# Kernel optimization log

Hardware: AMD Instinct MI355X
Metric: run time of the kernel (lower is better)

## Reference

```python
import jax, jax.numpy as jnp
import numpy as np
import math

N = 8192        # n_cells
D_IN = 512      # input_dim
D_H = 1024      # hidden_dim
N_F = 8         # min(8, N//2)
FS = N // N_F   # faction size
SYNC = 0.15
DEBATE = 0.15
TWO_PI = 2.0 * math.pi


def setup_inputs() -> dict:
    key = jax.random.key(0)
    ks = jax.random.split(key, 10)
    phases = jax.random.uniform(ks[0], (N,), dtype=jnp.float32) * TWO_PI
    omegas = jax.random.normal(ks[1], (N,), dtype=jnp.float32) * 0.5 + 1.0
    coupling = jax.random.normal(ks[2], (N, N), dtype=jnp.float32) * 0.01
    K = jnp.asarray(2.0, dtype=jnp.float32)
    # Linear weights stored as [in, out]
    w_p2h = jax.random.normal(ks[3], (2, D_H), dtype=jnp.float32) * (1.0 / math.sqrt(2.0))
    b_p2h = jnp.zeros((D_H,), dtype=jnp.float32)
    w_enc1 = jax.random.normal(ks[4], (D_H + D_IN, D_H), dtype=jnp.float32) * (1.0 / math.sqrt(D_H + D_IN))
    b_enc1 = jnp.zeros((D_H,), dtype=jnp.float32)
    w_enc2 = jax.random.normal(ks[5], (D_H, D_H), dtype=jnp.float32) * (1.0 / math.sqrt(D_H))
    b_enc2 = jnp.zeros((D_H,), dtype=jnp.float32)
    w_out = jax.random.normal(ks[6], (D_H, D_IN), dtype=jnp.float32) * (1.0 / math.sqrt(D_H))
    b_out = jnp.zeros((D_IN,), dtype=jnp.float32)
    x = jax.random.normal(ks[7], (D_IN,), dtype=jnp.float32)
    return {"x": x, "phases": phases, "omegas": omegas, "coupling": coupling, "K": K,
            "w_p2h": w_p2h, "b_p2h": b_p2h, "w_enc1": w_enc1, "b_enc1": b_enc1,
            "w_enc2": w_enc2, "b_enc2": b_enc2, "w_out": w_out, "b_out": b_out,
            "step": 10}


def _forward(x, phases, omegas, coupling, K, w_p2h, b_p2h, w_enc1, b_enc1,
             w_enc2, b_enc2, w_out, b_out, step):
    # --- kuramoto_step (torch runs it under no_grad) ---
    input_mag = jax.lax.stop_gradient(jnp.linalg.norm(x))
    phase_diff = phases[:, None] - phases[None, :]                 # [N, N]
    coupling_eff = jax.nn.sigmoid(coupling) * K / N                # [N, N]
    interactions = (coupling_eff * jnp.sin(phase_diff)).sum(axis=1)
    dtheta = omegas + interactions + input_mag * 0.1
    phases_new = jax.lax.stop_gradient((phases + 0.1 * dtheta) % TWO_PI)
    sin_p, cos_p = jnp.sin(phases_new), jnp.cos(phases_new)
    r = jnp.sqrt(cos_p.mean() ** 2 + sin_p.mean() ** 2)
    tension = jnp.abs(r - 0.5) * 2.0                               # scalar (non-diff, .item() in torch)

    # --- phase features -> per-cell hidden ---
    phase_features = jnp.stack([sin_p, cos_p], axis=-1)            # [N, 2]
    cell_hiddens = phase_features @ w_p2h + b_p2h                  # [N, D_H]

    # --- faction_sync_debate, vectorized over the 8 factions ---
    h = cell_hiddens.reshape(N_F, FS, D_H)
    fmean = h.mean(axis=1, keepdims=True)                          # [N_F, 1, D_H]
    h = (1.0 - SYNC) * h + SYNC * fmean
    if step > 5:  # step is a static Python int
        global_opinion = h.mean(axis=1).mean(axis=0)               # [D_H]
        dc = max(1, FS // 4)
        h = h.at[:, :dc].set((1.0 - DEBATE) * h[:, :dc] + DEBATE * global_opinion)
    cell_hiddens = h.reshape(N, D_H)

    # --- encode with broadcast input ---
    x_b = jnp.broadcast_to(x, (N, D_IN))
    combined = jnp.concatenate([cell_hiddens, x_b], axis=-1)       # [N, D_H + D_IN]
    encoded = jnp.tanh(combined @ w_enc1 + b_enc1) @ w_enc2 + b_enc2

    # --- coherence-weighted readout ---
    mean_phase = jnp.arctan2(sin_p.mean(), cos_p.mean())
    coherence = jnp.cos(phases_new - mean_phase)                   # [N]
    weights = jax.nn.softmax(coherence * 5.0)
    weighted = (weights[:, None] * encoded).sum(axis=0, keepdims=True)  # [1, D_H]
    output = weighted @ w_out + b_out                              # [1, D_IN]
    return output, tension


def reference(x, phases, omegas, coupling, K, w_p2h, b_p2h, w_enc1, b_enc1,
              w_enc2, b_enc2, w_out, b_out, step):
    return _forward(x, phases, omegas, coupling, K, w_p2h, b_p2h, w_enc1,
                    b_enc1, w_enc2, b_enc2, w_out, b_out, step)
```

## Files before the change

### kernel.cpp

```cpp
#include <hip/hip_runtime.h>
#include <math.h>


#define NC   8192
#define DH   1024
#define DIN  512

using f4 = __attribute__((ext_vector_type(4))) float;

constexpr int IMG = 0, SBAR = 1, CBAR = 2, MPC = 3, MPS = 4, DEN = 5, TENS = 6;
constexpr int SFO = 8, CFO = 16;
constexpr int SN0 = 32;
constexpr int CN0 = SN0 + NC;
constexpr int SNN = CN0 + NC;
constexpr int CNN = SNN + NC;
constexpr int UPART  = CNN + NC;
constexpr int UFIN   = UPART + 16 * 3 * DH;
constexpr int TPART  = UFIN + 3 * DH;
constexpr int W2PART = TPART + 128 * DH;
constexpr int OPART  = W2PART + 16 * DH;

__device__ __forceinline__ float frcp(float x) { return __builtin_amdgcn_rcpf(x); }
__device__ __forceinline__ float sigm(float x) { return frcp(1.f + __expf(-x)); }
__device__ __forceinline__ float ftanh(float x) { return 1.f - 2.f * frcp(__expf(2.f * x) + 1.f); }

template <int BS>
__device__ __forceinline__ float block_reduce(float v, float* sh) {
  #pragma unroll
  for (int m = 1; m < 64; m <<= 1) v += __shfl_xor(v, m, 64);
  constexpr int NW = BS / 64;
  int lane = threadIdx.x & 63, w = threadIdx.x >> 6;
  if (lane == 0) sh[w] = v;
  __syncthreads();
  if (w == 0) {
    float x = (lane < NW) ? sh[lane] : 0.f;
    #pragma unroll
    for (int m = 1; m < NW; m <<= 1) x += __shfl_xor(x, m, 64);
    if (lane == 0) sh[0] = x;
  }
  __syncthreads();
  float r = sh[0];
  __syncthreads();
  return r;
}

__global__ __launch_bounds__(256) void k_prep_up(const float* __restrict__ phases,
                                                 const float* __restrict__ x,
                                                 const float* __restrict__ w_p2h,
                                                 const float* __restrict__ b_p2h,
                                                 const float* __restrict__ w_enc1,
                                                 const float* __restrict__ b_enc1,
                                                 float* __restrict__ W) {
  __shared__ float sh[4];
  int b = blockIdx.x, t = threadIdx.x;
  if (b < 32) {
    int i = b * 256 + t;
    float s, c;
    sincosf(phases[i], &s, &c);
    W[SN0 + i] = s;
    W[CN0 + i] = c;
  } else if (b == 32) {
    float x0 = x[t], x1 = x[t + 256];
    float v = block_reduce<256>(x0 * x0 + x1 * x1, sh);
    if (t == 0) W[IMG] = sqrtf(v);
  } else {
    int idx = b - 33;
    int hb = idx & 3;
    int dy = idx >> 2;
    int h = hb * 256 + t;
    float a0 = 0.f, a1 = 0.f, a2 = 0.f;
    for (int d = dy * 64; d < dy * 64 + 64; ++d) {
      float r = w_enc1[d * DH + h];
      a0 = fmaf(w_p2h[d], r, a0);
      a1 = fmaf(w_p2h[DH + d], r, a1);
      a2 = fmaf(b_p2h[d], r, a2);
    }
    for (int k = dy * 32; k < dy * 32 + 32; ++k)
      a2 = fmaf(x[k], w_enc1[(DH + k) * DH + h], a2);
    if (dy == 0) a2 += b_enc1[h];
    float* up = W + UPART + dy * 3 * DH;
    up[h] = a0;
    up[DH + h] = a1;
    up[2 * DH + h] = a2;
  }
}

__global__ __launch_bounds__(256) void k_rows(const float* __restrict__ coupling,
                                              const float* __restrict__ phases,
                                              const float* __restrict__ omegas,
                                              const float* __restrict__ Kp,
                                              float* __restrict__ W) {
  __shared__ float sh[4][4];
  int t = threadIdx.x;
  int row0 = blockIdx.x * 2;
  const f4* c0 = (const f4*)(coupling + (size_t)row0 * NC);
  const f4* c1 = (const f4*)(coupling + (size_t)(row0 + 1) * NC);
  const f4* s4 = (const f4*)(W + SN0);
  const f4* c4 = (const f4*)(W + CN0);
  float sc0 = 0.f, ss0 = 0.f, sc1 = 0.f, ss1 = 0.f;
  #pragma unroll 4
  for (int k = 0; k < 8; ++k) {
    int idx = k * 256 + t;
    f4 cc = c4[idx];
    f4 sv = s4[idx];
    f4 v0 = __builtin_nontemporal_load(c0 + idx);
    f4 v1 = __builtin_nontemporal_load(c1 + idx);
    #pragma unroll
    for (int e = 0; e < 4; ++e) {
      float g0 = sigm(v0[e]);
      sc0 = fmaf(g0, cc[e], sc0);
      ss0 = fmaf(g0, sv[e], ss0);
      float g1 = sigm(v1[e]);
      sc1 = fmaf(g1, cc[e], sc1);
      ss1 = fmaf(g1, sv[e], ss1);
    }
  }
  #pragma unroll
  for (int m = 1; m < 64; m <<= 1) {
    sc0 += __shfl_xor(sc0, m, 64);
    ss0 += __shfl_xor(ss0, m, 64);
    sc1 += __shfl_xor(sc1, m, 64);
    ss1 += __shfl_xor(ss1, m, 64);
  }
  int lane = t & 63, w = t >> 6;
  if (lane == 0) { sh[w][0] = sc0; sh[w][1] = ss0; sh[w][2] = sc1; sh[w][3] = ss1; }
  __syncthreads();
  if (t < 2) {
    float sc = sh[0][2 * t] + sh[1][2 * t] + sh[2][2 * t] + sh[3][2 * t];
    float ss = sh[0][2 * t + 1] + sh[1][2 * t + 1] + sh[2][2 * t + 1] + sh[3][2 * t + 1];
    int row = row0 + t;
    float kk = Kp[0];
    float si = W[SN0 + row], ci = W[CN0 + row];
    float inter = (kk / (float)NC) * (si * sc - ci * ss);
    float dtheta = omegas[row] + inter + 0.1f * W[IMG];
    float pn = phases[row] + 0.1f * dtheta;
    float s, c;
    sincosf(pn, &s, &c);
    W[SNN + row] = s;
    W[CNN + row] = c;
  }
}

__global__ __launch_bounds__(1024) void k_stats_ured(float* __restrict__ W) {
  if (blockIdx.x > 0) {
    int j = (blockIdx.x - 1) * 1024 + threadIdx.x;
    float v = 0.f;
    #pragma unroll
    for (int p = 0; p < 16; ++p) v += W[UPART + p * 3 * DH + j];
    W[UFIN + j] = v;
    return;
  }
  __shared__ float shS[16], shC[16], shD[16], shMP[2];
  int t = threadIdx.x, lane = t & 63, w = t >> 6;
  int f = w >> 1, half = w & 1;
  int base = f * 1024 + half * 512;
  float s = 0.f, c = 0.f;
  #pragma unroll
  for (int k = 0; k < 8; ++k) {
    int i = base + k * 64 + lane;
    s += W[SNN + i];
    c += W[CNN + i];
  }
  #pragma unroll
  for (int m = 1; m < 64; m <<= 1) {
    s += __shfl_xor(s, m, 64);
    c += __shfl_xor(c, m, 64);
  }
  if (lane == 0) { shS[w] = s; shC[w] = c; }
  __syncthreads();
  if (t == 0) {
    float ssum = 0.f, csum = 0.f;
    #pragma unroll
    for (int ff = 0; ff < 8; ++ff) {
      float S = shS[2 * ff] + shS[2 * ff + 1];
      float C = shC[2 * ff] + shC[2 * ff + 1];
      W[SFO + ff] = S * (1.f / 1024.f);
      W[CFO + ff] = C * (1.f / 1024.f);
      ssum += S;
      csum += C;
    }
    float sbar = ssum * (1.f / (float)NC);
    float cbar = csum * (1.f / (float)NC);
    float mp = atan2f(sbar, cbar);
    float mpc = cosf(mp), mps = sinf(mp);
    W[SBAR] = sbar; W[CBAR] = cbar; W[MPC] = mpc; W[MPS] = mps;
    float r = sqrtf(cbar * cbar + sbar * sbar);
    W[TENS] = fabsf(r - 0.5f) * 2.f;
    shMP[0] = mpc; shMP[1] = mps;
  }
  __syncthreads();
  float mpc = shMP[0], mps = shMP[1];
  float d = 0.f;
  #pragma unroll
  for (int k = 0; k < 8; ++k) {
    int i = k * 1024 + t;
    float coh = W[CNN + i] * mpc + W[SNN + i] * mps;
    d += __expf(5.f * coh - 5.f);
  }
  #pragma unroll
  for (int m = 1; m < 64; m <<= 1) d += __shfl_xor(d, m, 64);
  if (lane == 0) shD[w] = d;
  __syncthreads();
  if (t == 0) {
    float D = 0.f;
    #pragma unroll
    for (int ww = 0; ww < 16; ++ww) D += shD[ww];
    W[DEN] = D;
  }
}

__global__ __launch_bounds__(256) void k_cells(const int* __restrict__ step,
                                               float* __restrict__ W) {
  int t = threadIdx.x, b = blockIdx.x;
  float u0[4], u1[4], u2[4], acc[4] = {0.f, 0.f, 0.f, 0.f};
  #pragma unroll
  for (int k = 0; k < 4; ++k) {
    int h = t + k * 256;
    u0[k] = W[UFIN + h];
    u1[k] = W[UFIN + DH + h];
    u2[k] = W[UFIN + 2 * DH + h];
  }
  bool debate = step[0] > 5;
  float sbar = W[SBAR], cbar = W[CBAR], mpc = W[MPC], mps = W[MPS];
  float invden = 1.0f / W[DEN];
  int i0 = b * 64;
  int f = i0 >> 10;
  float Sf = W[SFO + f], Cf = W[CFO + f];
  bool deb = debate && ((i0 & 1023) < 256);
  for (int j = 0; j < 64; ++j) {
    int i = i0 + j;
    float s = W[SNN + i], c = W[CNN + i];
    float a = fmaf(0.15f, Sf, 0.85f * s);
    float bb = fmaf(0.15f, Cf, 0.85f * c);
    if (deb) {
      a = fmaf(0.15f, sbar, 0.85f * a);
      bb = fmaf(0.15f, cbar, 0.85f * bb);
    }
    float coh = c * mpc + s * mps;
    float wgt = __expf(5.f * coh - 5.f) * invden;
    #pragma unroll
    for (int k = 0; k < 4; ++k) {
      float pre = fmaf(a, u0[k], fmaf(bb, u1[k], u2[k]));
      acc[k] = fmaf(wgt, ftanh(pre), acc[k]);
    }
  }
  #pragma unroll
  for (int k = 0; k < 4; ++k) W[TPART + b * DH + t + k * 256] = acc[k];
}

__global__ __launch_bounds__(256) void k_wv(const float* __restrict__ w_enc2,
                                            const float* __restrict__ b_enc2,
                                            float* __restrict__ W) {
  __shared__ float ts[64];
  int t = threadIdx.x, cb = blockIdx.x, hb = blockIdx.y;
  if (t < 64) {
    int h = hb * 64 + t;
    float v = 0.f;
    for (int p = 0; p < 128; ++p) v += W[TPART + p * DH + h];
    ts[t] = v;
  }
  __syncthreads();
  int c = cb * 256 + t;
  float acc = (hb == 0) ? b_enc2[c] : 0.f;
  #pragma unroll 8
  for (int j = 0; j < 64; ++j) acc = fmaf(ts[j], w_enc2[(hb * 64 + j) * DH + c], acc);
  W[W2PART + hb * DH + c] = acc;
}

__global__ __launch_bounds__(256) void k_out(const float* __restrict__ w_out,
                                             float* __restrict__ W) {
  __shared__ float wv[64];
  int t = threadIdx.x, ob = blockIdx.x, cb = blockIdx.y;
  if (t < 64) {
    int c = cb * 64 + t;
    float v = 0.f;
    #pragma unroll
    for (int p = 0; p < 16; ++p) v += W[W2PART + p * DH + c];
    wv[t] = v;
  }
  __syncthreads();
  int o = ob * 256 + t;
  float acc = 0.f;
  #pragma unroll 8
  for (int j = 0; j < 64; ++j) acc = fmaf(wv[j], w_out[(cb * 64 + j) * DIN + o], acc);
  W[OPART + cb * DIN + o] = acc;
}

__global__ __launch_bounds__(256) void k_final(const float* __restrict__ b_out,
                                               float* __restrict__ W,
                                               float* __restrict__ out) {
  int o = blockIdx.x * 256 + threadIdx.x;
  float acc = b_out[o];
  #pragma unroll
  for (int p = 0; p < 16; ++p) acc += W[OPART + p * DIN + o];
  out[o] = acc;
  if (o == 0) out[DIN] = W[TENS];
}

extern "C" void kernel_launch(void* const* d_in, const int* in_sizes, int n_in,
                              void* d_out, int out_size, void* d_ws, size_t ws_size,
                              hipStream_t stream) {
  (void)in_sizes; (void)n_in; (void)out_size; (void)ws_size;
  const float* x        = (const float*)d_in[0];
  const float* phases   = (const float*)d_in[1];
  const float* omegas   = (const float*)d_in[2];
  const float* coupling = (const float*)d_in[3];
  const float* Kp       = (const float*)d_in[4];
  const float* w_p2h    = (const float*)d_in[5];
  const float* b_p2h    = (const float*)d_in[6];
  const float* w_enc1   = (const float*)d_in[7];
  const float* b_enc1   = (const float*)d_in[8];
  const float* w_enc2   = (const float*)d_in[9];
  const float* b_enc2   = (const float*)d_in[10];
  const float* w_out    = (const float*)d_in[11];
  const float* b_out    = (const float*)d_in[12];
  const int*   step     = (const int*)d_in[13];
  float* W   = (float*)d_ws;
  float* out = (float*)d_out;

  k_prep_up   <<<97, 256, 0, stream>>>(phases, x, w_p2h, b_p2h, w_enc1, b_enc1, W);
  k_rows      <<<NC / 2, 256, 0, stream>>>(coupling, phases, omegas, Kp, W);
  k_stats_ured<<<4, 1024, 0, stream>>>(W);
  k_cells     <<<128, 256, 0, stream>>>(step, W);
  k_wv        <<<dim3(4, 16), 256, 0, stream>>>(w_enc2, b_enc2, W);
  k_out       <<<dim3(2, 16), 256, 0, stream>>>(w_out, W);
  k_final     <<<2, 256, 0, stream>>>(b_out, W, out);
}
```

Baseline: 88.86 us.

## Merge stats kernel into cells, fold weight prep into row pass, 8 rows per block

Removes the separate stats/u-reduction kernel. Every k_cells block now redundantly computes the faction sums, mean phase and softmax denominator over all 8192 cells, and sums the 16 u partials itself. The precomputation of w_enc1 projections moves from the prep kernel into the coupling-row kernel as 64 extra blocks, so it runs alongside the main memory-bound pass. The row kernel now handles 8 rows per block instead of 2, reusing the sin/cos vector loads across rows. This cuts one launch and a serial single-block stage, at the cost of redundant reductions in 128 blocks and higher register pressure in the row kernel.

Measured after the change: 108.1 us. 1.22x slower.

```diff
diff --git a/kernel.cpp b/kernel.cpp
--- a/kernel.cpp
+++ b/kernel.cpp
@@ -8,15 +8,13 @@
 
 using f4 = __attribute__((ext_vector_type(4))) float;
 
-constexpr int IMG = 0, SBAR = 1, CBAR = 2, MPC = 3, MPS = 4, DEN = 5, TENS = 6;
-constexpr int SFO = 8, CFO = 16;
+constexpr int IMG = 0, TENS = 6;
 constexpr int SN0 = 32;
 constexpr int CN0 = SN0 + NC;
 constexpr int SNN = CN0 + NC;
 constexpr int CNN = SNN + NC;
 constexpr int UPART  = CNN + NC;
-constexpr int UFIN   = UPART + 16 * 3 * DH;
-constexpr int TPART  = UFIN + 3 * DH;
+constexpr int TPART  = UPART + 16 * 3 * DH;
 constexpr int W2PART = TPART + 128 * DH;
 constexpr int OPART  = W2PART + 16 * DH;
 
@@ -24,33 +22,9 @@
 __device__ __forceinline__ float sigm(float x) { return frcp(1.f + __expf(-x)); }
 __device__ __forceinline__ float ftanh(float x) { return 1.f - 2.f * frcp(__expf(2.f * x) + 1.f); }
 
-template <int BS>
-__device__ __forceinline__ float block_reduce(float v, float* sh) {
-  #pragma unroll
-  for (int m = 1; m < 64; m <<= 1) v += __shfl_xor(v, m, 64);
-  constexpr int NW = BS / 64;
-  int lane = threadIdx.x & 63, w = threadIdx.x >> 6;
-  if (lane == 0) sh[w] = v;
-  __syncthreads();
-  if (w == 0) {
-    float x = (lane < NW) ? sh[lane] : 0.f;
-    #pragma unroll
-    for (int m = 1; m < NW; m <<= 1) x += __shfl_xor(x, m, 64);
-    if (lane == 0) sh[0] = x;
-  }
-  __syncthreads();
-  float r = sh[0];
-  __syncthreads();
-  return r;
-}
-
-__global__ __launch_bounds__(256) void k_prep_up(const float* __restrict__ phases,
-                                                 const float* __restrict__ x,
-                                                 const float* __restrict__ w_p2h,
-                                                 const float* __restrict__ b_p2h,
-                                                 const float* __restrict__ w_enc1,
-                                                 const float* __restrict__ b_enc1,
-                                                 float* __restrict__ W) {
+__global__ __launch_bounds__(256) void k_prep(const float* __restrict__ phases,
+                                              const float* __restrict__ x,
+                                              float* __restrict__ W) {
   __shared__ float sh[4];
   int b = blockIdx.x, t = threadIdx.x;
   if (b < 32) {
@@ -59,12 +33,31 @@
     sincosf(phases[i], &s, &c);
     W[SN0 + i] = s;
     W[CN0 + i] = c;
-  } else if (b == 32) {
+  } else {
     float x0 = x[t], x1 = x[t + 256];
-    float v = block_reduce<256>(x0 * x0 + x1 * x1, sh);
-    if (t == 0) W[IMG] = sqrtf(v);
-  } else {
-    int idx = b - 33;
+    float v = x0 * x0 + x1 * x1;
+    #pragma unroll
+    for (int m = 1; m < 64; m <<= 1) v += __shfl_xor(v, m, 64);
+    int lane = t & 63, w = t >> 6;
+    if (lane == 0) sh[w] = v;
+    __syncthreads();
+    if (t == 0) W[IMG] = sqrtf(sh[0] + sh[1] + sh[2] + sh[3]);
+  }
+}
+
+__global__ __launch_bounds__(256) void k_rows_up(const float* __restrict__ coupling,
+                                                 const float* __restrict__ phases,
+                                                 const float* __restrict__ omegas,
+                                                 const float* __restrict__ Kp,
+                                                 const float* __restrict__ x,
+                                                 const float* __restrict__ w_p2h,
+                                                 const float* __restrict__ b_p2h,
+                                                 const float* __restrict__ w_enc1,
+                                                 const float* __restrict__ b_enc1,
+                                                 float* __restrict__ W) {
+  int t = threadIdx.x;
+  if (blockIdx.x < 64) {
+    int idx = blockIdx.x;
     int hb = idx & 3;
     int dy = idx >> 2;
     int h = hb * 256 + t;
@@ -82,56 +75,52 @@
     up[h] = a0;
     up[DH + h] = a1;
     up[2 * DH + h] = a2;
-  }
-}
-
-__global__ __launch_bounds__(256) void k_rows(const float* __restrict__ coupling,
-                                              const float* __restrict__ phases,
-                                              const float* __restrict__ omegas,
-                                              const float* __restrict__ Kp,
-                                              float* __restrict__ W) {
-  __shared__ float sh[4][4];
-  int t = threadIdx.x;
-  int row0 = blockIdx.x * 2;
-  const f4* c0 = (const f4*)(coupling + (size_t)row0 * NC);
-  const f4* c1 = (const f4*)(coupling + (size_t)(row0 + 1) * NC);
+    return;
+  }
+  __shared__ float sh[4][16];
+  int row0 = (blockIdx.x - 64) * 8;
+  const f4* cbase = (const f4*)(coupling + (size_t)row0 * NC);
   const f4* s4 = (const f4*)(W + SN0);
   const f4* c4 = (const f4*)(W + CN0);
-  float sc0 = 0.f, ss0 = 0.f, sc1 = 0.f, ss1 = 0.f;
-  #pragma unroll 4
+  float sc[8], ss[8];
+  #pragma unroll
+  for (int r = 0; r < 8; ++r) { sc[r] = 0.f; ss[r] = 0.f; }
   for (int k = 0; k < 8; ++k) {
     int idx = k * 256 + t;
     f4 cc = c4[idx];
     f4 sv = s4[idx];
-    f4 v0 = __builtin_nontemporal_load(c0 + idx);
-    f4 v1 = __builtin_nontemporal_load(c1 + idx);
-    #pragma unroll
-    for (int e = 0; e < 4; ++e) {
-      float g0 = sigm(v0[e]);
-      sc0 = fmaf(g0, cc[e], sc0);
-      ss0 = fmaf(g0, sv[e], ss0);
-      float g1 = sigm(v1[e]);
-      sc1 = fmaf(g1, cc[e], sc1);
-      ss1 = fmaf(g1, sv[e], ss1);
-    }
-  }
-  #pragma unroll
-  for (int m = 1; m < 64; m <<= 1) {
-    sc0 += __shfl_xor(sc0, m, 64);
-    ss0 += __shfl_xor(ss0, m, 64);
-    sc1 += __shfl_xor(sc1, m, 64);
-    ss1 += __shfl_xor(ss1, m, 64);
+    #pragma unroll
+    for (int r = 0; r < 8; ++r) {
+      f4 v = __builtin_nontemporal_load(cbase + r * (NC / 4) + idx);
+      #pragma unroll
+      for (int e = 0; e < 4; ++e) {
+        float g = sigm(v[e]);
+        sc[r] = fmaf(g, cc[e], sc[r]);
+        ss[r] = fmaf(g, sv[e], ss[r]);
+      }
+    }
   }
   int lane = t & 63, w = t >> 6;
-  if (lane == 0) { sh[w][0] = sc0; sh[w][1] = ss0; sh[w][2] = sc1; sh[w][3] = ss1; }
-  __syncthreads();
-  if (t < 2) {
-    float sc = sh[0][2 * t] + sh[1][2 * t] + sh[2][2 * t] + sh[3][2 * t];
-    float ss = sh[0][2 * t + 1] + sh[1][2 * t + 1] + sh[2][2 * t + 1] + sh[3][2 * t + 1];
+  #pragma unroll
+  for (int r = 0; r < 8; ++r) {
+    #pragma unroll
+    for (int m = 1; m < 64; m <<= 1) {
+      sc[r] += __shfl_xor(sc[r], m, 64);
+      ss[r] += __shfl_xor(ss[r], m, 64);
+    }
+  }
+  if (lane == 0) {
+    #pragma unroll
+    for (int r = 0; r < 8; ++r) { sh[w][2 * r] = sc[r]; sh[w][2 * r + 1] = ss[r]; }
+  }
+  __syncthreads();
+  if (t < 8) {
+    float scf = sh[0][2 * t] + sh[1][2 * t] + sh[2][2 * t] + sh[3][2 * t];
+    float ssf = sh[0][2 * t + 1] + sh[1][2 * t + 1] + sh[2][2 * t + 1] + sh[3][2 * t + 1];
     int row = row0 + t;
     float kk = Kp[0];
     float si = W[SN0 + row], ci = W[CN0 + row];
-    float inter = (kk / (float)NC) * (si * sc - ci * ss);
+    float inter = (kk / (float)NC) * (si * scf - ci * ssf);
     float dtheta = omegas[row] + inter + 0.1f * W[IMG];
     float pn = phases[row] + 0.1f * dtheta;
     float s, c;
@@ -141,91 +130,94 @@
   }
 }
 
-__global__ __launch_bounds__(1024) void k_stats_ured(float* __restrict__ W) {
-  if (blockIdx.x > 0) {
-    int j = (blockIdx.x - 1) * 1024 + threadIdx.x;
-    float v = 0.f;
-    #pragma unroll
-    for (int p = 0; p < 16; ++p) v += W[UPART + p * 3 * DH + j];
-    W[UFIN + j] = v;
-    return;
-  }
-  __shared__ float shS[16], shC[16], shD[16], shMP[2];
-  int t = threadIdx.x, lane = t & 63, w = t >> 6;
-  int f = w >> 1, half = w & 1;
-  int base = f * 1024 + half * 512;
-  float s = 0.f, c = 0.f;
-  #pragma unroll
-  for (int k = 0; k < 8; ++k) {
-    int i = base + k * 64 + lane;
-    s += W[SNN + i];
-    c += W[CNN + i];
-  }
-  #pragma unroll
-  for (int m = 1; m < 64; m <<= 1) {
-    s += __shfl_xor(s, m, 64);
-    c += __shfl_xor(c, m, 64);
-  }
-  if (lane == 0) { shS[w] = s; shC[w] = c; }
+__global__ __launch_bounds__(256) void k_cells(const int* __restrict__ step,
+                                               float* __restrict__ W) {
+  __shared__ float shS[4][8], shC[4][8], shD[4];
+  __shared__ float bcS[8], bcC[8], bc2[6];
+  int t = threadIdx.x, b = blockIdx.x;
+  int lane = t & 63, w = t >> 6;
+  const f4* s4 = (const f4*)(W + SNN);
+  const f4* c4 = (const f4*)(W + CNN);
+  float sp[8], cp[8];
+  #pragma unroll
+  for (int f = 0; f < 8; ++f) {
+    f4 sv = s4[f * 256 + t];
+    f4 cv = c4[f * 256 + t];
+    sp[f] = (sv[0] + sv[1]) + (sv[2] + sv[3]);
+    cp[f] = (cv[0] + cv[1]) + (cv[2] + cv[3]);
+  }
+  #pragma unroll
+  for (int f = 0; f < 8; ++f) {
+    #pragma unroll
+    for (int m = 1; m < 64; m <<= 1) {
+      sp[f] += __shfl_xor(sp[f], m, 64);
+      cp[f] += __shfl_xor(cp[f], m, 64);
+    }
+  }
+  if (lane == 0) {
+    #pragma unroll
+    for (int f = 0; f < 8; ++f) { shS[w][f] = sp[f]; shC[w][f] = cp[f]; }
+  }
   __syncthreads();
   if (t == 0) {
     float ssum = 0.f, csum = 0.f;
     #pragma unroll
-    for (int ff = 0; ff < 8; ++ff) {
-      float S = shS[2 * ff] + shS[2 * ff + 1];
-      float C = shC[2 * ff] + shC[2 * ff + 1];
-      W[SFO + ff] = S * (1.f / 1024.f);
-      W[CFO + ff] = C * (1.f / 1024.f);
+    for (int f = 0; f < 8; ++f) {
+      float S = (shS[0][f] + shS[1][f]) + (shS[2][f] + shS[3][f]);
+      float C = (shC[0][f] + shC[1][f]) + (shC[2][f] + shC[3][f]);
+      bcS[f] = S * (1.f / 1024.f);
+      bcC[f] = C * (1.f / 1024.f);
       ssum += S;
       csum += C;
     }
     float sbar = ssum * (1.f / (float)NC);
     float cbar = csum * (1.f / (float)NC);
     float mp = atan2f(sbar, cbar);
-    float mpc = cosf(mp), mps = sinf(mp);
-    W[SBAR] = sbar; W[CBAR] = cbar; W[MPC] = mpc; W[MPS] = mps;
-    float r = sqrtf(cbar * cbar + sbar * sbar);
-    W[TENS] = fabsf(r - 0.5f) * 2.f;
-    shMP[0] = mpc; shMP[1] = mps;
-  }
-  __syncthreads();
-  float mpc = shMP[0], mps = shMP[1];
+    bc2[0] = sbar; bc2[1] = cbar; bc2[2] = cosf(mp); bc2[3] = sinf(mp);
+    if (b == 0) {
+      float r = sqrtf(cbar * cbar + sbar * sbar);
+      W[TENS] = fabsf(r - 0.5f) * 2.f;
+    }
+  }
+  __syncthreads();
+  float mpc = bc2[2], mps = bc2[3];
   float d = 0.f;
   #pragma unroll
   for (int k = 0; k < 8; ++k) {
-    int i = k * 1024 + t;
-    float coh = W[CNN + i] * mpc + W[SNN + i] * mps;
-    d += __expf(5.f * coh - 5.f);
+    f4 sv = s4[k * 256 + t];
+    f4 cv = c4[k * 256 + t];
+    #pragma unroll
+    for (int e = 0; e < 4; ++e) {
+      float coh = cv[e] * mpc + sv[e] * mps;
+      d += __expf(5.f * coh - 5.f);
+    }
   }
   #pragma unroll
   for (int m = 1; m < 64; m <<= 1) d += __shfl_xor(d, m, 64);
   if (lane == 0) shD[w] = d;
   __syncthreads();
-  if (t == 0) {
-    float D = 0.f;
-    #pragma unroll
-    for (int ww = 0; ww < 16; ++ww) D += shD[ww];
-    W[DEN] = D;
-  }
-}
-
-__global__ __launch_bounds__(256) void k_cells(const int* __restrict__ step,
-                                               float* __restrict__ W) {
-  int t = threadIdx.x, b = blockIdx.x;
+  if (t == 0) bc2[4] = 1.0f / ((shD[0] + shD[1]) + (shD[2] + shD[3]));
+  __syncthreads();
+  float invden = bc2[4];
+  float sbar = bc2[0], cbar = bc2[1];
   float u0[4], u1[4], u2[4], acc[4] = {0.f, 0.f, 0.f, 0.f};
   #pragma unroll
   for (int k = 0; k < 4; ++k) {
     int h = t + k * 256;
-    u0[k] = W[UFIN + h];
-    u1[k] = W[UFIN + DH + h];
-    u2[k] = W[UFIN + 2 * DH + h];
+    float v0 = 0.f, v1 = 0.f, v2 = 0.f;
+    #pragma unroll
+    for (int p = 0; p < 16; ++p) {
+      const float* up = W + UPART + p * 3 * DH;
+      v0 += up[h];
+      v1 += up[DH + h];
+      v2 += up[2 * DH + h];
+    }
+    u0[k] = v0; u1[k] = v1; u2[k] = v2;
   }
   bool debate = step[0] > 5;
-  float sbar = W[SBAR], cbar = W[CBAR], mpc = W[MPC], mps = W[MPS];
-  float invden = 1.0f / W[DEN];
   int i0 = b * 64;
   int f = i0 >> 10;
-  float Sf = W[SFO + f], Cf = W[CFO + f];
+  float Sf = bcS[f], Cf = bcC[f];
   bool deb = debate && ((i0 & 1023) < 256);
   for (int j = 0; j < 64; ++j) {
     int i = i0 + j;
@@ -318,11 +310,11 @@
   float* W   = (float*)d_ws;
   float* out = (float*)d_out;
 
-  k_prep_up   <<<97, 256, 0, stream>>>(phases, x, w_p2h, b_p2h, w_enc1, b_enc1, W);
-  k_rows      <<<NC / 2, 256, 0, stream>>>(coupling, phases, omegas, Kp, W);
-  k_stats_ured<<<4, 1024, 0, stream>>>(W);
-  k_cells     <<<128, 256, 0, stream>>>(step, W);
-  k_wv        <<<dim3(4, 16), 256, 0, stream>>>(w_enc2, b_enc2, W);
-  k_out       <<<dim3(2, 16), 256, 0, stream>>>(w_out, W);
-  k_final     <<<2, 256, 0, stream>>>(b_out, W, out);
-}
+  k_prep   <<<33, 256, 0, stream>>>(phases, x, W);
+  k_rows_up<<<64 + NC / 8, 256, 0, stream>>>(coupling, phases, omegas, Kp,
+                                             x, w_p2h, b_p2h, w_enc1, b_enc1, W);
+  k_cells  <<<128, 256, 0, stream>>>(step, W);
+  k_wv     <<<dim3(4, 16), 256, 0, stream>>>(w_enc2, b_enc2, W);
+  k_out    <<<dim3(2, 16), 256, 0, stream>>>(w_out, W);
+  k_final  <<<2, 256, 0, stream>>>(b_out, W, out);
+}
```

## Fuse final reduction into k_out via atomic counter and vectorize prep kernel

Applied to the files above, without the earlier changes.

Removes the separate k_final launch: each k_out block bumps a counter in the workspace (zeroed in k_wv), and the last block to arrive sums the partial outputs and writes the result. The prep kernel now uses float4 loads and stores for the w_enc1 projection, so each thread covers four hidden columns and the grid shrinks from 97 to 49 blocks. The aim is to save one kernel launch and widen memory transactions. The cost is less parallelism in the prep stage and an atomic/acquire-release handshake at the end of k_out.

After: 91.05 us. +2.5%, slower.

```diff
diff --git a/kernel.cpp b/kernel.cpp
--- a/kernel.cpp
+++ b/kernel.cpp
@@ -8,8 +8,7 @@
 
 using f4 = __attribute__((ext_vector_type(4))) float;
 
-constexpr int IMG = 0, SBAR = 1, CBAR = 2, MPC = 3, MPS = 4, DEN = 5, TENS = 6;
-constexpr int SFO = 8, CFO = 16;
+constexpr int IMG = 0, TENS = 6, CNT = 7;
 constexpr int SN0 = 32;
 constexpr int CN0 = SN0 + NC;
 constexpr int SNN = CN0 + NC;
@@ -64,24 +63,33 @@
     float v = block_reduce<256>(x0 * x0 + x1 * x1, sh);
     if (t == 0) W[IMG] = sqrtf(v);
   } else {
-    int idx = b - 33;
-    int hb = idx & 3;
-    int dy = idx >> 2;
-    int h = hb * 256 + t;
-    float a0 = 0.f, a1 = 0.f, a2 = 0.f;
+    int dy = b - 33;
+    f4 a0 = {0.f, 0.f, 0.f, 0.f}, a1 = a0, a2 = a0;
     for (int d = dy * 64; d < dy * 64 + 64; ++d) {
-      float r = w_enc1[d * DH + h];
-      a0 = fmaf(w_p2h[d], r, a0);
-      a1 = fmaf(w_p2h[DH + d], r, a1);
-      a2 = fmaf(b_p2h[d], r, a2);
-    }
-    for (int k = dy * 32; k < dy * 32 + 32; ++k)
-      a2 = fmaf(x[k], w_enc1[(DH + k) * DH + h], a2);
-    if (dy == 0) a2 += b_enc1[h];
+      f4 r = *(const f4*)(w_enc1 + (size_t)d * DH + 4 * t);
+      float s0 = w_p2h[d], s1 = w_p2h[DH + d], s2 = b_p2h[d];
+      #pragma unroll
+      for (int e = 0; e < 4; ++e) {
+        a0[e] = fmaf(s0, r[e], a0[e]);
+        a1[e] = fmaf(s1, r[e], a1[e]);
+        a2[e] = fmaf(s2, r[e], a2[e]);
+      }
+    }
+    for (int k = dy * 32; k < dy * 32 + 32; ++k) {
+      f4 r = *(const f4*)(w_enc1 + (size_t)(DH + k) * DH + 4 * t);
+      float xv = x[k];
+      #pragma unroll
+      for (int e = 0; e < 4; ++e) a2[e] = fmaf(xv, r[e], a2[e]);
+    }
+    if (dy == 0) {
+      f4 bb = *(const f4*)(b_enc1 + 4 * t);
+      #pragma unroll
+      for (int e = 0; e < 4; ++e) a2[e] += bb[e];
+    }
     float* up = W + UPART + dy * 3 * DH;
-    up[h] = a0;
-    up[DH + h] = a1;
-    up[2 * DH + h] = a2;
+    *(f4*)(up + 4 * t) = a0;
+    *(f4*)(up + DH + 4 * t) = a1;
+    *(f4*)(up + 2 * DH + 4 * t) = a2;
   }
 }
 
@@ -174,8 +182,8 @@
     for (int ff = 0; ff < 8; ++ff) {
       float S = shS[2 * ff] + shS[2 * ff + 1];
       float C = shC[2 * ff] + shC[2 * ff + 1];
-      W[SFO + ff] = S * (1.f / 1024.f);
-      W[CFO + ff] = C * (1.f / 1024.f);
+      W[8 + ff] = S * (1.f / 1024.f);
+      W[16 + ff] = C * (1.f / 1024.f);
       ssum += S;
       csum += C;
     }
@@ -183,7 +191,7 @@
     float cbar = csum * (1.f / (float)NC);
     float mp = atan2f(sbar, cbar);
     float mpc = cosf(mp), mps = sinf(mp);
-    W[SBAR] = sbar; W[CBAR] = cbar; W[MPC] = mpc; W[MPS] = mps;
+    W[1] = sbar; W[2] = cbar; W[3] = mpc; W[4] = mps;
     float r = sqrtf(cbar * cbar + sbar * sbar);
     W[TENS] = fabsf(r - 0.5f) * 2.f;
     shMP[0] = mpc; shMP[1] = mps;
@@ -205,7 +213,7 @@
     float D = 0.f;
     #pragma unroll
     for (int ww = 0; ww < 16; ++ww) D += shD[ww];
-    W[DEN] = D;
+    W[5] = D;
   }
 }
 
@@ -221,11 +229,11 @@
     u2[k] = W[UFIN + 2 * DH + h];
   }
   bool debate = step[0] > 5;
-  float sbar = W[SBAR], cbar = W[CBAR], mpc = W[MPC], mps = W[MPS];
-  float invden = 1.0f / W[DEN];
+  float sbar = W[1], cbar = W[2], mpc = W[3], mps = W[4];
+  float invden = 1.0f / W[5];
   int i0 = b * 64;
   int f = i0 >> 10;
-  float Sf = W[SFO + f], Cf = W[CFO + f];
+  float Sf = W[8 + f], Cf = W[16 + f];
   bool deb = debate && ((i0 & 1023) < 256);
   for (int j = 0; j < 64; ++j) {
     int i = i0 + j;
@@ -253,6 +261,7 @@
                                             float* __restrict__ W) {
   __shared__ float ts[64];
   int t = threadIdx.x, cb = blockIdx.x, hb = blockIdx.y;
+  if (t == 0 && cb == 0 && hb == 0) *(unsigned*)(W + CNT) = 0u;
   if (t < 64) {
     int h = hb * 64 + t;
     float v = 0.f;
@@ -268,8 +277,11 @@
 }
 
 __global__ __launch_bounds__(256) void k_out(const float* __restrict__ w_out,
-                                             float* __restrict__ W) {
+                                             const float* __restrict__ b_out,
+                                             float* __restrict__ W,
+                                             float* __restrict__ out) {
   __shared__ float wv[64];
+  __shared__ int last;
   int t = threadIdx.x, ob = blockIdx.x, cb = blockIdx.y;
   if (t < 64) {
     int c = cb * 64 + t;
@@ -284,17 +296,21 @@
   #pragma unroll 8
   for (int j = 0; j < 64; ++j) acc = fmaf(wv[j], w_out[(cb * 64 + j) * DIN + o], acc);
   W[OPART + cb * DIN + o] = acc;
-}
-
-__global__ __launch_bounds__(256) void k_final(const float* __restrict__ b_out,
-                                               float* __restrict__ W,
-                                               float* __restrict__ out) {
-  int o = blockIdx.x * 256 + threadIdx.x;
-  float acc = b_out[o];
-  #pragma unroll
-  for (int p = 0; p < 16; ++p) acc += W[OPART + p * DIN + o];
-  out[o] = acc;
-  if (o == 0) out[DIN] = W[TENS];
+  __syncthreads();
+  if (t == 0) {
+    unsigned old = __hip_atomic_fetch_add((unsigned*)(W + CNT), 1u,
+                                          __ATOMIC_ACQ_REL, __HIP_MEMORY_SCOPE_AGENT);
+    last = (old == 31u);
+  }
+  __syncthreads();
+  if (!last) return;
+  for (int oo = t; oo < DIN; oo += 256) {
+    float a = b_out[oo];
+    #pragma unroll
+    for (int p = 0; p < 16; ++p) a += W[OPART + p * DIN + oo];
+    out[oo] = a;
+  }
+  if (t == 0) out[DIN] = W[TENS];
 }
 
 extern "C" void kernel_launch(void* const* d_in, const int* in_sizes, int n_in,
@@ -318,11 +334,10 @@
   float* W   = (float*)d_ws;
   float* out = (float*)d_out;
 
-  k_prep_up   <<<97, 256, 0, stream>>>(phases, x, w_p2h, b_p2h, w_enc1, b_enc1, W);
+  k_prep_up   <<<49, 256, 0, stream>>>(phases, x, w_p2h, b_p2h, w_enc1, b_enc1, W);
   k_rows      <<<NC / 2, 256, 0, stream>>>(coupling, phases, omegas, Kp, W);
   k_stats_ured<<<4, 1024, 0, stream>>>(W);
   k_cells     <<<128, 256, 0, stream>>>(step, W);
   k_wv        <<<dim3(4, 16), 256, 0, stream>>>(w_enc2, b_enc2, W);
-  k_out       <<<dim3(2, 16), 256, 0, stream>>>(w_out, W);
-  k_final     <<<2, 256, 0, stream>>>(b_out, W, out);
-}
+  k_out       <<<dim3(2, 16), 256, 0, stream>>>(w_out, b_out, W, out);
+}
```
